# Kernel tuning notes

Hardware: AMD Instinct MI355X
Metric: run time of the kernel (lower is better)

The kernel has to match this reference:

```python
import jax, jax.numpy as jnp
import numpy as np

B, L, WD, H = 16, 48, 1024, 1024
RANK_H = 128
TEMP = 1.0


def setup_inputs():
    key = jax.random.key(0)
    ks = jax.random.split(key, 10)
    se = jax.random.normal(ks[0], (B, L, WD), jnp.float32)
    length = jnp.clip(jax.random.randint(ks[1], (B,), 8, L + 1), 2, L)
    gumbel_u = jax.random.uniform(ks[2], (B, L), jnp.float32, minval=1e-6, maxval=1.0 - 1e-6)
    sc = 0.02
    Wih = jax.random.normal(ks[3], (4 * H, WD), jnp.float32) * sc
    Whh = jax.random.normal(ks[4], (4 * H, H), jnp.float32) * sc
    bih = jnp.zeros((4 * H,), jnp.float32).at[H:2 * H].set(1.0)  # forget-gate bias = 1
    bhh = jnp.zeros((4 * H,), jnp.float32)
    R1 = jax.random.normal(ks[5], (RANK_H, H), jnp.float32) * 0.01  # rank Linear 1 (no bias)
    R2 = jax.random.normal(ks[6], (1, RANK_H), jnp.float32) * 0.01  # rank Linear 2 (no bias)
    Wc = jax.random.normal(ks[7], (6 * H, 3 * H), jnp.float32) * sc  # Nary compose linear
    bc = jnp.zeros((6 * H,), jnp.float32)
    return dict(sentence_embedding=se, gumbel_u=gumbel_u, Wih=Wih, Whh=Whh,
                bih=bih, bhh=bhh, R1=R1, R2=R2, Wc=Wc, bc=bc, length=length)


def leaf_lstm(x, Wih, Whh, bih, bhh):
    # torch.nn.LSTMCell over time; x: [B, L, WD] -> hs, cs: [B, L, H]
    h0 = jnp.zeros((x.shape[0], H), x.dtype)

    def step(carry, xt):
        h, c = carry
        g = xt @ Wih.T + bih + h @ Whh.T + bhh
        i, f, u, o = jnp.split(g, 4, axis=-1)  # torch gate order i, f, g, o
        c = jax.nn.sigmoid(f) * c + jax.nn.sigmoid(i) * jnp.tanh(u)
        h = jax.nn.sigmoid(o) * jnp.tanh(c)
        return (h, c), (h, c)

    _, (hs, cs) = jax.lax.scan(step, (h0, h0), jnp.swapaxes(x, 0, 1))
    return jnp.swapaxes(hs, 0, 1), jnp.swapaxes(cs, 0, 1)


def nary_cell(lh, lc, rh, rc, xh, xc, Wc, bc):
    # 3-ary tree-LSTM composition: gates i, f_left, f_right, f_x, u, o
    g = jnp.concatenate([lh, rh, xh], axis=-1) @ Wc.T + bc
    i, fl, fr, fx, u, o = jnp.split(g, 6, axis=-1)
    c = (jax.nn.sigmoid(i) * jnp.tanh(u) + jax.nn.sigmoid(fl) * lc
         + jax.nn.sigmoid(fr) * rc + jax.nn.sigmoid(fx) * xc)
    h = jax.nn.sigmoid(o) * jnp.tanh(c)
    return h, c


def build(hs, cs, noise, start, end, R1, R2, Wc, bc):
    # hs, cs: [L, H] for one sentence; returns (h, c) each [H]
    if end <= start:
        z = jnp.zeros((H,), hs.dtype)
        return z, z
    if end == start + 1:
        return hs[start], cs[start]
    x = jax.lax.stop_gradient(hs[start:end])          # rank_detach=True
    s = (jax.nn.relu(x @ R1.T) @ R2.T)[:, 0]          # rank MLP scores [n]
    pos = start + int(jnp.argmax(s))                  # split point = noiseless argmax
    soft = jax.nn.softmax((s + noise[start:end]) / TEMP)
    hard = jax.nn.one_hot(int(jnp.argmax(soft)), end - start, dtype=soft.dtype)
    gate = soft + jax.lax.stop_gradient(hard - soft)  # straight-through gumbel-softmax
    h = gate @ hs[start:end]
    c = gate @ cs[start:end]
    lh, lc = build(hs, cs, noise, start, pos, R1, R2, Wc, bc)
    rh, rc = build(hs, cs, noise, pos + 1, end, R1, R2, Wc, bc)
    return nary_cell(lh, lc, rh, rc, h, c, Wc, bc)


def reference(sentence_embedding, gumbel_u, Wih, Whh, bih, bhh, R1, R2, Wc, bc, length):
    noise = -jnp.log(-jnp.log(gumbel_u))  # Gumbel(0, 1) noise
    hs, cs = leaf_lstm(sentence_embedding, Wih, Whh, bih, bhh)
    lens = [int(v) for v in np.asarray(length)]
    h_res, c_res = [], []
    for b in range(B):
        h, c = build(hs[b], cs[b], noise[b], 0, lens[b], R1, R2, Wc, bc)
        h_res.append(h)
        c_res.append(c)
    return jnp.stack([jnp.stack(h_res), jnp.stack(c_res)])  # [2, B, H]
```

## Files before the change

kernel.cpp:

```cpp
#include <hip/hip_runtime.h>
#include <math.h>

#define BB 16
#define LL 48
#define HH 1024
#define NG4 4096
#define NG6 6144
#define K3H 3072
#define RANKH 128
#define MAXN 47
#define TOTN (BB*MAXN)
#define MAXLVL 48
#define MAXNPL 384

#define FSTRIDE 32
#define FDOM 8192
#define HS_S 1028

typedef __attribute__((ext_vector_type(8))) short bf16x8;
typedef __attribute__((ext_vector_type(4))) float f32x4;

__device__ __forceinline__ float sigf(float x){ return 1.f/(1.f + expf(-x)); }

__device__ __forceinline__ unsigned short f2bf(float f){
  union { float f; unsigned u; } v; v.f = f;
  unsigned r = v.u + 0x7fff + ((v.u >> 16) & 1);
  return (unsigned short)(r >> 16);
}

__device__ __forceinline__ void st_llc(float* p, float v){
  __hip_atomic_store(p, v, __ATOMIC_RELAXED, __HIP_MEMORY_SCOPE_AGENT);
}
__device__ __forceinline__ float ld_llc(const float* p){
  return __hip_atomic_load(p, __ATOMIC_RELAXED, __HIP_MEMORY_SCOPE_AGENT);
}
__device__ __forceinline__ void st_llc_u16(unsigned short* p, unsigned v){
  asm volatile("global_store_short %0, %1, off sc0 sc1" :: "v"(p), "v"(v) : "memory");
}
__device__ __forceinline__ void st_llc_u32(unsigned* p, unsigned v){
  asm volatile("global_store_dword %0, %1, off sc0 sc1" :: "v"(p), "v"(v) : "memory");
}
__device__ __forceinline__ void wait_vm0(){
  asm volatile("s_waitcnt vmcnt(0)" ::: "memory");
}

__device__ __forceinline__ void flagbar(unsigned* flags, unsigned p){
  wait_vm0();
  __syncthreads();
  int tid = threadIdx.x;
  if (tid == 0)
    st_llc_u32(&flags[blockIdx.x*FSTRIDE], p);
  for (;;){
    unsigned v;
    asm volatile("global_load_dword %0, %1, off sc0 sc1"
                 : "=v"(v) : "v"(&flags[tid*FSTRIDE]));
    wait_vm0();
    if (__all((int)(v >= p))) break;
  }
  __syncthreads();
}

__global__ __launch_bounds__(256) void k_init(unsigned* flags, unsigned short* zrow){
  int tid = threadIdx.x;
  for (int i = tid; i < 2*FDOM; i += 256) flags[i] = 0u;
  for (int i = tid; i < 1024; i += 256) zrow[i] = 0;
}

__global__ __launch_bounds__(256) void k_cvt_bf16(const float* __restrict__ in,
    unsigned short* __restrict__ out, int n){
  int i = (blockIdx.x*256 + threadIdx.x)*4;
  if (i >= n) return;
  float4 v = *(const float4*)(in + i);
  ushort4 o;
  o.x = f2bf(v.x); o.y = f2bf(v.y); o.z = f2bf(v.z); o.w = f2bf(v.w);
  *(ushort4*)(out + i) = o;
}

__global__ __launch_bounds__(256) void k_transpose(const float* __restrict__ in,
                                                   float* __restrict__ out, int R, int C){
  __shared__ float t[32][33];
  int bx = blockIdx.x*32, by = blockIdx.y*32;
  int x = threadIdx.x, y = threadIdx.y;
  #pragma unroll
  for (int i = 0; i < 32; i += 8){
    int r = by + y + i, c = bx + x;
    if (r < R && c < C) t[y+i][x] = in[(size_t)r*C + c];
  }
  __syncthreads();
  #pragma unroll
  for (int i = 0; i < 32; i += 8){
    int r = bx + y + i, c = by + x;
    if (r < C && c < R) out[(size_t)r*R + c] = t[x][y+i];
  }
}

__global__ __launch_bounds__(256) void k_gemm_gx(const float* __restrict__ A,
    const float* __restrict__ Bw, const float* __restrict__ bih,
    const float* __restrict__ bhh, float* __restrict__ Cout, int M, int N, int K){
  __shared__ float as[16][68];
  __shared__ float bs[16][68];
  int m0 = blockIdx.x*64, n0 = blockIdx.y*64;
  int tid = threadIdx.x;
  int mt = tid & 15, nt = tid >> 4;
  float acc[4][4] = {};
  for (int k0 = 0; k0 < K; k0 += 16){
    #pragma unroll
    for (int it = 0; it < 4; ++it){
      int idx = it*256 + tid;
      int kk = idx & 15, mm = idx >> 4;
      as[kk][mm] = A[(size_t)(m0+mm)*K + k0 + kk];
      bs[kk][mm] = Bw[(size_t)(n0+mm)*K + k0 + kk];
    }
    __syncthreads();
    #pragma unroll
    for (int kk = 0; kk < 16; ++kk){
      float a4[4], b4[4];
      #pragma unroll
      for (int i = 0; i < 4; ++i) a4[i] = as[kk][mt*4+i];
      #pragma unroll
      for (int i = 0; i < 4; ++i) b4[i] = bs[kk][nt*4+i];
      #pragma unroll
      for (int i = 0; i < 4; ++i)
        #pragma unroll
        for (int j2 = 0; j2 < 4; ++j2) acc[i][j2] += a4[i]*b4[j2];
    }
    __syncthreads();
  }
  #pragma unroll
  for (int i = 0; i < 4; ++i){
    int m = m0 + mt*4 + i;
    #pragma unroll
    for (int j2 = 0; j2 < 4; ++j2){
      int n = n0 + nt*4 + j2;
      Cout[(size_t)m*N + n] = acc[i][j2] + bih[n] + bhh[n];
    }
  }
}

__global__ __launch_bounds__(256) void k_gx_t(const float* __restrict__ Gx,
                                              float* __restrict__ Gxt){
  __shared__ float t2[16][257];
  int t = blockIdx.x;
  int rc = blockIdx.y;
  int tid = threadIdx.x;
  #pragma unroll
  for (int m = 0; m < 16; ++m)
    t2[m][tid] = Gx[((size_t)(m*48 + t))*4096 + rc*256 + tid];
  __syncthreads();
  int rl = tid >> 4, m = tid & 15;
  #pragma unroll
  for (int i = 0; i < 16; ++i){
    int r = rc*256 + i*16 + rl;
    Gxt[((size_t)t*4096 + r)*16 + m] = t2[m][i*16 + rl];
  }
}

__global__ __launch_bounds__(256, 1) void k_lstm_scan(
    const float* __restrict__ Whh, const float* __restrict__ Gxt,
    float* __restrict__ hx,
    float* __restrict__ hs, float* __restrict__ cs,
    unsigned short* __restrict__ hs_bf, unsigned* __restrict__ flags){
  __shared__ float smem[17408];
  __shared__ float gbuf[4*64];
  __shared__ float cbuf[64];
  int tid = threadIdx.x;
  int g = tid >> 6, kc = tid & 63;
  int j0 = blockIdx.x * 4;
  float w[4][16];
  #pragma unroll
  for (int jj = 0; jj < 4; ++jj){
    const float* src = Whh + (size_t)(g*1024 + j0 + jj)*1024 + kc*4;
    #pragma unroll
    for (int r = 0; r < 4; ++r){
      float4 v = *(const float4*)(src + r*256);
      w[jj][r*4+0]=v.x; w[jj][r*4+1]=v.y; w[jj][r*4+2]=v.z; w[jj][r*4+3]=v.w;
    }
  }
  if (tid < 64) cbuf[tid] = 0.f;
  for (int t = 0; t < LL; ++t){
    float gx = Gxt[((size_t)t*NG4 + g*1024 + j0 + (kc & 3))*16 + (kc >> 2)];
    float G = 0.f;
    if (t > 0){
      const float* slab = hx + (size_t)(t-1)*16384;
      f32x4 hv[16];
      #pragma unroll
      for (int i = 0; i < 16; ++i)
        hv[i] = *(const f32x4*)(slab + i*1024 + tid*4);
      {
        int mb = (tid & 3) * 4;
        int jb = tid >> 2;
        #pragma unroll
        for (int i = 0; i < 16; ++i){
          #pragma unroll
          for (int e = 0; e < 4; ++e)
            smem[(size_t)(mb + e)*HS_S + i*64 + jb] = hv[i][e];
        }
      }
      __syncthreads();
      float acc[4][16];
      #pragma unroll 4
      for (int m = 0; m < 16; ++m){
        const float* hb = &smem[(size_t)m*HS_S + (kc<<2)];
        float4 h0 = *(const float4*)(hb);
        float4 h1 = *(const float4*)(hb+256);
        float4 h2 = *(const float4*)(hb+512);
        float4 h3 = *(const float4*)(hb+768);
        #pragma unroll
        for (int jj = 0; jj < 4; ++jj){
          float s = w[jj][0]*h0.x + w[jj][1]*h0.y + w[jj][2]*h0.z + w[jj][3]*h0.w
                  + w[jj][4]*h1.x + w[jj][5]*h1.y + w[jj][6]*h1.z + w[jj][7]*h1.w
                  + w[jj][8]*h2.x + w[jj][9]*h2.y + w[jj][10]*h2.z + w[jj][11]*h2.w
                  + w[jj][12]*h3.x + w[jj][13]*h3.y + w[jj][14]*h3.z + w[jj][15]*h3.w;
          acc[jj][m] = s;
        }
      }
      __syncthreads();
      #pragma unroll
      for (int m = 0; m < 16; ++m){
        float4 v;
        v.x = acc[0][m]; v.y = acc[1][m]; v.z = acc[2][m]; v.w = acc[3][m];
        *(float4*)&smem[(size_t)(g*64 + kc)*68 + m*4] = v;
      }
      __syncthreads();
      {
        float s0=0.f,s1=0.f,s2=0.f,s3=0.f;
        #pragma unroll 4
        for (int l = 0; l < 64; l += 4){
          s0 += smem[(size_t)(g*64 + l  )*68 + kc];
          s1 += smem[(size_t)(g*64 + l+1)*68 + kc];
          s2 += smem[(size_t)(g*64 + l+2)*68 + kc];
          s3 += smem[(size_t)(g*64 + l+3)*68 + kc];
        }
        G = (s0+s1)+(s2+s3);
      }
    }
    gbuf[g*64 + kc] = G + gx;
    __syncthreads();
    if (g == 0){
      int o = kc;
      int jj = o >> 4, m = o & 15;
      int op = m*4 + jj;
      float gi = gbuf[0*64 + op];
      float gf = gbuf[1*64 + op];
      float gu = gbuf[2*64 + op];
      float go = gbuf[3*64 + op];
      float cp = cbuf[op];
      float c = sigf(gf)*cp + sigf(gi)*tanhf(gu);
      float h = sigf(go)*tanhf(c);
      cbuf[op] = c;
      st_llc(&hx[(size_t)t*16384 + j0*16 + o], h);
      size_t oidx = ((size_t)(m*LL + t))*HH + j0 + jj;
      hs[oidx] = h;
      cs[oidx] = c;
      hs_bf[oidx] = f2bf(h);
    }
    if (t < LL-1)
      flagbar(flags, (unsigned)(t+1));
  }
}

__global__ __launch_bounds__(128) void k_score(const float* __restrict__ R1t,
    const float* __restrict__ R2, const float* __restrict__ hs,
    const float* __restrict__ gumbel_u, float* __restrict__ score,
    float* __restrict__ snoisy){
  __shared__ float hsm[HH];
  __shared__ float red[128];
  int bt = blockIdx.x;
  int tid = threadIdx.x;
  for (int i = tid; i < HH; i += 128) hsm[i] = hs[(size_t)bt*HH + i];
  __syncthreads();
  float acc = 0.f;
  for (int k = 0; k < HH; ++k) acc += R1t[(size_t)k*RANKH + tid] * hsm[k];
  red[tid] = fmaxf(acc, 0.f) * R2[tid];
  __syncthreads();
  for (int s = 64; s > 0; s >>= 1){
    if (tid < s) red[tid] += red[tid+s];
    __syncthreads();
  }
  if (tid == 0){
    float s = red[0];
    float u = gumbel_u[bt];
    float noise = -logf(-logf(u));
    score[bt]  = s;
    snoisy[bt] = s + noise;
  }
}

__global__ __launch_bounds__(64) void k_build(const float* __restrict__ score,
    const float* __restrict__ snoisy, const int* __restrict__ length,
    int* __restrict__ node_l, int* __restrict__ node_r, int* __restrict__ node_x,
    int* __restrict__ node_lvl, int* __restrict__ node_b, int* __restrict__ node_root,
    int* __restrict__ level_count, int* __restrict__ level_off, int* __restrict__ order){
  __shared__ float sc[BB*LL], sn[BB*LL];
  __shared__ int lcount[MAXLVL+1], lcur[MAXLVL+1], loff[MAXLVL+1];
  __shared__ int percnt[BB];
  int tid = threadIdx.x;
  for (int i = tid; i < BB*LL; i += 64){ sc[i] = score[i]; sn[i] = snoisy[i]; }
  for (int i = tid; i <= MAXLVL; i += 64){ lcount[i] = 0; lcur[i] = 0; }
  __syncthreads();
  if (tid < BB){
    int b = tid;
    int len = length[b];
    if (len > LL) len = LL;
    int qs[MAXN], qe[MAXN], qn[MAXN];
    int qh = 0, qt = 0, cnt = 0;
    int rootn = cnt++;
    qs[qt] = 0; qe[qt] = len; qn[qt] = rootn; qt++;
    while (qh < qt){
      int s0 = qs[qh], e0 = qe[qh], nid = qn[qh]; qh++;
      float best = sc[b*LL + s0]; int pos = s0;
      for (int t2 = s0+1; t2 < e0; ++t2){
        float v = sc[b*LL + t2];
        if (v > best){ best = v; pos = t2; }
      }
      float bestn = sn[b*LL + s0]; int js = s0;
      for (int t2 = s0+1; t2 < e0; ++t2){
        float v = sn[b*LL + t2];
        if (v > bestn){ bestn = v; js = t2; }
      }
      int gid = b*MAXN + nid;
      node_x[gid] = js;
      node_b[gid] = b;
      node_root[gid] = (nid == 0) ? 1 : 0;
      int ln = pos - s0, enc_l, enc_r;
      if (ln <= 0) enc_l = -1;
      else if (ln == 1) enc_l = 10000 + s0;
      else { int c2 = cnt++; enc_l = b*MAXN + c2; qs[qt]=s0; qe[qt]=pos; qn[qt]=c2; qt++; }
      int rn = e0 - (pos+1);
      if (rn <= 0) enc_r = -1;
      else if (rn == 1) enc_r = 10000 + (pos+1);
      else { int c2 = cnt++; enc_r = b*MAXN + c2; qs[qt]=pos+1; qe[qt]=e0; qn[qt]=c2; qt++; }
      node_l[gid] = enc_l; node_r[gid] = enc_r;
    }
    for (int i = cnt-1; i >= 0; --i){
      int gid = b*MAXN + i;
      int el = node_l[gid], er = node_r[gid];
      int llv = (el >= 0 && el < 10000) ? node_lvl[el] : 0;
      int rlv = (er >= 0 && er < 10000) ? node_lvl[er] : 0;
      node_lvl[gid] = 1 + (llv > rlv ? llv : rlv);
    }
    for (int i = 0; i < cnt; ++i) atomicAdd(&lcount[node_lvl[b*MAXN + i]], 1);
    percnt[b] = cnt;
  }
  __syncthreads();
  if (tid == 0){
    int off = 0, nlev = 0;
    for (int lv = 1; lv <= MAXLVL; ++lv){
      loff[lv] = off;
      level_off[lv] = off;
      level_count[lv] = lcount[lv];
      if (lcount[lv] > 0) nlev = lv;
      off += lcount[lv];
    }
    level_count[0] = nlev;
  }
  __syncthreads();
  if (tid < BB){
    int b = tid;
    int cnt = percnt[b];
    for (int i = 0; i < cnt; ++i){
      int gid = b*MAXN + i;
      int lv = node_lvl[gid];
      int p = atomicAdd(&lcur[lv], 1);
      order[loff[lv] + p] = gid;
    }
  }
}

__global__ __launch_bounds__(256, 1) void k_tree(
    const unsigned short* __restrict__ Wc_bf,
    const unsigned short* __restrict__ hs_bf,
    unsigned short* __restrict__ nodeH_bf,
    const unsigned short* __restrict__ zrow,
    const float* __restrict__ bc, const float* __restrict__ cs,
    float* __restrict__ nodeC,
    const int* __restrict__ node_l, const int* __restrict__ node_r,
    const int* __restrict__ node_x, const int* __restrict__ node_b,
    const int* __restrict__ node_root, const int* __restrict__ level_count,
    const int* __restrict__ level_off, const int* __restrict__ order,
    float* __restrict__ gates, float* __restrict__ out,
    unsigned* __restrict__ flags){
  __shared__ __align__(16) unsigned char wlds[24*6144];
  int tid = threadIdx.x;
  int lane = tid & 63;
  int wave = tid >> 6;
  int fr = lane & 15;
  int fkq = lane >> 4;
  int fk  = fkq * 8;
  int fkb = fkq * 16;
  int swz = (fr & 7) << 4;
  int base0 = fr * 6144;
  int base1 = (16 + (fr & 7)) * 6144;
  int rg24 = blockIdx.x * 24;

  for (int i = tid; i < 24*384; i += 256){
    int row = i / 384;
    int ch  = i - row*384;
    uint4 v = *(const uint4*)(Wc_bf + (size_t)(rg24 + row)*K3H + ch*8);
    *(uint4*)(wlds + row*6144 + ((ch*16) ^ ((row & 7) << 4))) = v;
  }
  __syncthreads();

  int nlev = level_count[0];
  unsigned ph = 0;
  for (int lvl = 1; lvl <= nlev; ++lvl){
    int n = level_count[lvl];
    int loffv = level_off[lvl];
    int mtiles = (n + 15) >> 4;
    for (int mt = wave; mt < mtiles; mt += 4){
      int slot = mt*16 + fr;
      const unsigned short *pa0, *pa1, *pa2;
      if (slot < n){
        int gid = order[loffv + slot];
        int b = node_b[gid];
        int el = node_l[gid], er = node_r[gid], xt = node_x[gid];
        pa0 = (el < 0) ? zrow : (el >= 10000 ? hs_bf + (size_t)(b*LL + (el-10000))*HH
                                             : nodeH_bf + (size_t)el*HH);
        pa1 = (er < 0) ? zrow : (er >= 10000 ? hs_bf + (size_t)(b*LL + (er-10000))*HH
                                             : nodeH_bf + (size_t)er*HH);
        pa2 = hs_bf + (size_t)(b*LL + xt)*HH;
      } else { pa0 = zrow; pa1 = zrow; pa2 = zrow; }
      const unsigned short* pa[3] = {pa0, pa1, pa2};
      f32x4 acc0 = {0.f,0.f,0.f,0.f};
      f32x4 acc1 = {0.f,0.f,0.f,0.f};
      #pragma unroll
      for (int part = 0; part < 3; ++part){
        const unsigned short* ap = pa[part] + fk;
        #pragma unroll 8
        for (int kcc = 0; kcc < 1024; kcc += 32){
          bf16x8 a = *(const bf16x8*)(ap + kcc);
          int xb = part*2048 + kcc*2 + fkb;
          bf16x8 b0 = *(const bf16x8*)(wlds + base0 + (xb ^ swz));
          bf16x8 b1 = *(const bf16x8*)(wlds + base1 + (xb ^ swz));
          acc0 = __builtin_amdgcn_mfma_f32_16x16x32_bf16(a, b0, acc0, 0, 0, 0);
          acc1 = __builtin_amdgcn_mfma_f32_16x16x32_bf16(a, b1, acc1, 0, 0, 0);
        }
      }
      int m0 = mt*16 + fkq*4;
      #pragma unroll
      for (int r = 0; r < 4; ++r){
        int m = m0 + r;
        if (m < n){
          st_llc(&gates[(size_t)m*NG6 + rg24 + fr], acc0[r]);
          if (fr < 8)
            st_llc(&gates[(size_t)m*NG6 + rg24 + 16 + fr], acc1[r]);
        }
      }
    }
    ph++;
    flagbar(flags, ph);
    int items = n * 4;
    for (int it = blockIdx.x; it < items; it += 256){
      int ns = it >> 2;
      int j = (it & 3)*256 + tid;
      int gid = order[loffv + ns];
      int b = node_b[gid];
      int el = node_l[gid], er = node_r[gid], xt = node_x[gid];
      float gg[6];
      #pragma unroll
      for (int q = 0; q < 6; ++q)
        gg[q] = bc[q*HH + j] + ld_llc(&gates[(size_t)ns*NG6 + q*HH + j]);
      float lc = (el < 0) ? 0.f : (el >= 10000 ? cs[(size_t)(b*LL + (el-10000))*HH + j]
                                               : nodeC[(size_t)el*HH + j]);
      float rc = (er < 0) ? 0.f : (er >= 10000 ? cs[(size_t)(b*LL + (er-10000))*HH + j]
                                               : nodeC[(size_t)er*HH + j]);
      float xc = cs[(size_t)(b*LL + xt)*HH + j];
      float c = sigf(gg[0])*tanhf(gg[4]) + sigf(gg[1])*lc + sigf(gg[2])*rc + sigf(gg[3])*xc;
      float h = sigf(gg[5])*tanhf(c);
      st_llc_u16(&nodeH_bf[(size_t)gid*HH + j], (unsigned)f2bf(h));
      st_llc(&nodeC[(size_t)gid*HH + j], c);
      if (node_root[gid]){
        out[(size_t)b*HH + j] = h;
        out[(size_t)BB*HH + (size_t)b*HH + j] = c;
      }
    }
    if (lvl < nlev){
      ph++;
      flagbar(flags, ph);
    }
  }
}

extern "C" void kernel_launch(void* const* d_in, const int* in_sizes, int n_in,
                              void* d_out, int out_size, void* d_ws, size_t ws_size,
                              hipStream_t stream){
  const float* se  = (const float*)d_in[0];
  const float* gu  = (const float*)d_in[1];
  const float* Wih = (const float*)d_in[2];
  const float* Whh = (const float*)d_in[3];
  const float* bih = (const float*)d_in[4];
  const float* bhh = (const float*)d_in[5];
  const float* R1  = (const float*)d_in[6];
  const float* R2  = (const float*)d_in[7];
  const float* Wc  = (const float*)d_in[8];
  const float* bc  = (const float*)d_in[9];
  const int*   len = (const int*)d_in[10];
  float* out = (float*)d_out;

  float* ws = (float*)d_ws;
  size_t off = 0;
  float* R1t   = ws + off; off += (size_t)HH*RANKH;
  float* Gx    = ws + off; off += (size_t)BB*LL*NG4;
  float* Gxt   = ws + off; off += (size_t)BB*LL*NG4;
  float* hx    = ws + off; off += (size_t)LL*HH*BB;
  float* hs    = ws + off; off += (size_t)BB*LL*HH;
  float* cs    = ws + off; off += (size_t)BB*LL*HH;
  float* nodeC = ws + off; off += (size_t)TOTN*HH;
  float* gates = ws + off; off += (size_t)MAXNPL*NG6;
  unsigned short* Wc_bf    = (unsigned short*)(ws + off); off += (size_t)NG6*K3H/2;
  unsigned short* hs_bf    = (unsigned short*)(ws + off); off += (size_t)BB*LL*HH/2;
  unsigned short* nodeH_bf = (unsigned short*)(ws + off); off += (size_t)TOTN*HH/2 + 512;
  unsigned short* zrow     = (unsigned short*)(ws + off); off += 512;
  float* score = ws + off; off += 1024;
  float* snoi  = ws + off; off += 1024;
  unsigned* flags = (unsigned*)(ws + off); off += 2*FDOM;
  int* ib = (int*)(ws + off);
  int* node_l    = ib; ib += 768;
  int* node_r    = ib; ib += 768;
  int* node_x    = ib; ib += 768;
  int* node_lvl  = ib; ib += 768;
  int* node_b    = ib; ib += 768;
  int* node_root = ib; ib += 768;
  int* level_count = ib; ib += 64;
  int* level_off   = ib; ib += 64;
  int* order       = ib; ib += 768;

  k_init<<<1, 256, 0, stream>>>(flags, zrow);
  k_transpose<<<dim3(32, 4), dim3(32, 8), 0, stream>>>(R1, R1t, RANKH, HH);
  k_cvt_bf16<<<(NG6*K3H)/1024, 256, 0, stream>>>(Wc, Wc_bf, NG6*K3H);
  k_gemm_gx<<<dim3(12, 64), 256, 0, stream>>>(se, Wih, bih, bhh, Gx, BB*LL, NG4, HH);
  k_gx_t<<<dim3(48, 16), 256, 0, stream>>>(Gx, Gxt);
  k_lstm_scan<<<256, 256, 0, stream>>>(Whh, Gxt, hx, hs, cs, hs_bf, flags);
  k_score<<<BB*LL, 128, 0, stream>>>(R1t, R2, hs, gu, score, snoi);
  k_build<<<1, 64, 0, stream>>>(score, snoi, len, node_l, node_r, node_x,
                                node_lvl, node_b, node_root,
                                level_count, level_off, order);
  k_tree<<<256, 256, 0, stream>>>(Wc_bf, hs_bf, nodeH_bf, zrow, bc, cs, nodeC,
                                  node_l, node_r, node_x, node_b, node_root,
                                  level_count, level_off, order,
                                  gates, out, flags + FDOM);
}
```

Before: 1.035 ms.

## Merge preprocessing kernels, pad LSTM reduction buffer, defer output stores past barrier

Three small preprocessing launches (flag/zero init, R1 transpose, Wc bf16 conversion) are combined into one kernel that picks its role from the block index, removing two launches. In the LSTM scan, the partial-sum reduction buffer stride changes from 68 to 65 floats to cut LDS bank conflicts, giving up the vectorized float4 stores. The hs/cs/hs_bf global stores move after the inter-block flag barrier so they no longer delay the critical-path synchronization.

```diff
diff --git a/kernel.cpp b/kernel.cpp
--- a/kernel.cpp
+++ b/kernel.cpp
@@ -16,6 +16,9 @@
 #define FSTRIDE 32
 #define FDOM 8192
 #define HS_S 1028
+#define RED_S 65
+
+#define NB_CVT 18432
 
 typedef __attribute__((ext_vector_type(8))) short bf16x8;
 typedef __attribute__((ext_vector_type(4))) float f32x4;
@@ -60,37 +63,37 @@
   __syncthreads();
 }
 
-__global__ __launch_bounds__(256) void k_init(unsigned* flags, unsigned short* zrow){
-  int tid = threadIdx.x;
-  for (int i = tid; i < 2*FDOM; i += 256) flags[i] = 0u;
-  for (int i = tid; i < 1024; i += 256) zrow[i] = 0;
-}
-
-__global__ __launch_bounds__(256) void k_cvt_bf16(const float* __restrict__ in,
-    unsigned short* __restrict__ out, int n){
-  int i = (blockIdx.x*256 + threadIdx.x)*4;
-  if (i >= n) return;
-  float4 v = *(const float4*)(in + i);
-  ushort4 o;
-  o.x = f2bf(v.x); o.y = f2bf(v.y); o.z = f2bf(v.z); o.w = f2bf(v.w);
-  *(ushort4*)(out + i) = o;
-}
-
-__global__ __launch_bounds__(256) void k_transpose(const float* __restrict__ in,
-                                                   float* __restrict__ out, int R, int C){
-  __shared__ float t[32][33];
-  int bx = blockIdx.x*32, by = blockIdx.y*32;
-  int x = threadIdx.x, y = threadIdx.y;
-  #pragma unroll
-  for (int i = 0; i < 32; i += 8){
-    int r = by + y + i, c = bx + x;
-    if (r < R && c < C) t[y+i][x] = in[(size_t)r*C + c];
-  }
-  __syncthreads();
-  #pragma unroll
-  for (int i = 0; i < 32; i += 8){
-    int r = bx + y + i, c = by + x;
-    if (r < C && c < R) out[(size_t)r*R + c] = t[x][y+i];
+__global__ __launch_bounds__(256) void k_pre(const float* __restrict__ Wc,
+    unsigned short* __restrict__ Wc_bf, const float* __restrict__ R1,
+    float* __restrict__ R1t, unsigned* __restrict__ flags,
+    unsigned short* __restrict__ zrow){
+  __shared__ float tz[32][33];
+  int bid = blockIdx.x;
+  int tid = threadIdx.x;
+  if (bid < NB_CVT){
+    int i = (bid*256 + tid)*4;
+    float4 v = *(const float4*)(Wc + i);
+    ushort4 o;
+    o.x = f2bf(v.x); o.y = f2bf(v.y); o.z = f2bf(v.z); o.w = f2bf(v.w);
+    *(ushort4*)(Wc_bf + i) = o;
+  } else if (bid < NB_CVT + 128){
+    int id = bid - NB_CVT;
+    int bx = (id & 31)*32, by = (id >> 5)*32;
+    int x = tid & 31, y = tid >> 5;
+    #pragma unroll
+    for (int i = 0; i < 32; i += 8){
+      int r = by + y + i, c = bx + x;
+      if (r < RANKH && c < HH) tz[y+i][x] = R1[(size_t)r*HH + c];
+    }
+    __syncthreads();
+    #pragma unroll
+    for (int i = 0; i < 32; i += 8){
+      int r = bx + y + i, c = by + x;
+      if (r < HH && c < RANKH) R1t[(size_t)r*RANKH + c] = tz[x][y+i];
+    }
+  } else {
+    for (int i = tid; i < 2*FDOM; i += 256) flags[i] = 0u;
+    for (int i = tid; i < 1024; i += 256) zrow[i] = 0;
   }
 }
 
@@ -217,25 +220,27 @@
       __syncthreads();
       #pragma unroll
       for (int m = 0; m < 16; ++m){
-        float4 v;
-        v.x = acc[0][m]; v.y = acc[1][m]; v.z = acc[2][m]; v.w = acc[3][m];
-        *(float4*)&smem[(size_t)(g*64 + kc)*68 + m*4] = v;
+        #pragma unroll
+        for (int jj = 0; jj < 4; ++jj)
+          smem[(size_t)(g*64 + kc)*RED_S + m*4 + jj] = acc[jj][m];
       }
       __syncthreads();
       {
         float s0=0.f,s1=0.f,s2=0.f,s3=0.f;
         #pragma unroll 4
         for (int l = 0; l < 64; l += 4){
-          s0 += smem[(size_t)(g*64 + l  )*68 + kc];
-          s1 += smem[(size_t)(g*64 + l+1)*68 + kc];
-          s2 += smem[(size_t)(g*64 + l+2)*68 + kc];
-          s3 += smem[(size_t)(g*64 + l+3)*68 + kc];
+          s0 += smem[(size_t)(g*64 + l  )*RED_S + kc];
+          s1 += smem[(size_t)(g*64 + l+1)*RED_S + kc];
+          s2 += smem[(size_t)(g*64 + l+2)*RED_S + kc];
+          s3 += smem[(size_t)(g*64 + l+3)*RED_S + kc];
         }
         G = (s0+s1)+(s2+s3);
       }
     }
     gbuf[g*64 + kc] = G + gx;
     __syncthreads();
+    float hval = 0.f, cval = 0.f;
+    size_t oidx = 0;
     if (g == 0){
       int o = kc;
       int jj = o >> 4, m = o & 15;
@@ -245,17 +250,19 @@
       float gu = gbuf[2*64 + op];
       float go = gbuf[3*64 + op];
       float cp = cbuf[op];
-      float c = sigf(gf)*cp + sigf(gi)*tanhf(gu);
-      float h = sigf(go)*tanhf(c);
-      cbuf[op] = c;
-      st_llc(&hx[(size_t)t*16384 + j0*16 + o], h);
-      size_t oidx = ((size_t)(m*LL + t))*HH + j0 + jj;
-      hs[oidx] = h;
-      cs[oidx] = c;
-      hs_bf[oidx] = f2bf(h);
+      cval = sigf(gf)*cp + sigf(gi)*tanhf(gu);
+      hval = sigf(go)*tanhf(cval);
+      cbuf[op] = cval;
+      st_llc(&hx[(size_t)t*16384 + j0*16 + o], hval);
+      oidx = ((size_t)(m*LL + t))*HH + j0 + jj;
     }
     if (t < LL-1)
       flagbar(flags, (unsigned)(t+1));
+    if (g == 0){
+      hs[oidx] = hval;
+      cs[oidx] = cval;
+      hs_bf[oidx] = f2bf(hval);
+    }
   }
 }
 
@@ -525,9 +532,7 @@
   int* level_off   = ib; ib += 64;
   int* order       = ib; ib += 768;
 
-  k_init<<<1, 256, 0, stream>>>(flags, zrow);
-  k_transpose<<<dim3(32, 4), dim3(32, 8), 0, stream>>>(R1, R1t, RANKH, HH);
-  k_cvt_bf16<<<(NG6*K3H)/1024, 256, 0, stream>>>(Wc, Wc_bf, NG6*K3H);
+  k_pre<<<NB_CVT + 128 + 1, 256, 0, stream>>>(Wc, Wc_bf, R1, R1t, flags, zrow);
   k_gemm_gx<<<dim3(12, 64), 256, 0, stream>>>(se, Wih, bih, bhh, Gx, BB*LL, NG4, HH);
   k_gx_t<<<dim3(48, 16), 256, 0, stream>>>(Gx, Gxt);
   k_lstm_scan<<<256, 256, 0, stream>>>(Whh, Gxt, hx, hs, cs, hs_bf, flags);
```

New measurement: 1.021 ms (median of 2 runs). No clear change (-1.4%).
